# Optimization experiments

Measured on AMD Instinct MI355X. Metric: run time of the kernel, lower is better.

## Reference

```python
import jax, jax.numpy as jnp
from jax import lax
import numpy as np

COST_CLASS = 1.0
COST_BEZIER = 5.0
INF = jnp.float32(1e30)


def setup_inputs() -> dict:
    key = jax.random.key(0)
    k1, k2, k3, k4 = jax.random.split(key, 4)
    B, N, M, C = 16, 256, 256, 4096
    return {
        'pred_ctrl': jax.random.normal(k1, (B, N, 4, 2), dtype=jnp.float32),
        'pred_logits': jax.random.normal(k2, (B, N, C), dtype=jnp.float32),
        'gt_ctrl': jax.random.normal(k3, (B, M, 4, 2), dtype=jnp.float32),
        'gt_labels': jax.random.randint(k4, (B, M), 0, C, dtype=jnp.int64),
    }


def build_cost(pred_ctrl, pred_logits, gt_ctrl, gt_labels):
    B, N = pred_ctrl.shape[:2]
    M = gt_ctrl.shape[1]
    prob = jax.nn.softmax(pred_logits, axis=-1)                      # (B,N,C)
    lbl = jnp.broadcast_to(gt_labels[:, None, :], (B, N, M))          # (B,N,M)
    cost_class = -jnp.take_along_axis(prob, lbl, axis=2)              # (B,N,M)
    p = pred_ctrl.reshape(B, N, 8)
    g = gt_ctrl.reshape(B, M, 8)
    cost_bezier = jnp.sum(jnp.abs(p[:, :, None, :] - g[:, None, :, :]), axis=-1)  # L1 cdist
    return COST_CLASS * cost_class + COST_BEZIER * cost_bezier        # (B,N,M)


def lsa(cost):
    """Jonker-Volgenant shortest augmenting path, square n x n cost.
    Returns (row_ind, col_ind) matching scipy.optimize.linear_sum_assignment."""
    n = cost.shape[0]
    ar = jnp.arange(n)

    def solve_row(carry, cur_row):
        u, v, row4col, col4row = carry

        def cond(s):
            return s['sink'] < 0

        def body(s):
            i = s['i']
            SR = s['SR'].at[i].set(True)
            r = s['minVal'] + cost[i] - u[i] - v
            better = (r < s['spc']) & (~s['SC'])
            path = jnp.where(better, i, s['path'])
            spc = jnp.where(better, r, s['spc'])
            masked = jnp.where(s['SC'], INF, spc)
            j = jnp.argmin(masked).astype(jnp.int32)
            minVal = masked[j]
            SC = s['SC'].at[j].set(True)
            hit_free = row4col[j] < 0
            sink = jnp.where(hit_free, j, jnp.int32(-1))
            i_next = jnp.where(hit_free, i, row4col[j])
            return dict(i=i_next, minVal=minVal, SR=SR, SC=SC, spc=spc, path=path, sink=sink)

        init = dict(i=cur_row.astype(jnp.int32), minVal=jnp.float32(0),
                    SR=jnp.zeros(n, bool), SC=jnp.zeros(n, bool),
                    spc=jnp.full(n, INF), path=jnp.full(n, -1, jnp.int32),
                    sink=jnp.int32(-1))
        s = lax.while_loop(cond, body, init)
        minVal, SR, SC, spc, path, sink = s['minVal'], s['SR'], s['SC'], s['spc'], s['path'], s['sink']

        # dual updates
        u = u.at[cur_row].add(minVal)
        safe = jnp.clip(col4row, 0, n - 1)
        u = jnp.where(SR & (ar != cur_row), u + minVal - spc[safe], u)
        v = jnp.where(SC, v - (minVal - spc), v)

        # augment along predecessor path
        def aug_cond(t):
            return ~t['done']

        def aug_body(t):
            j = t['j']
            i = path[j]
            r4c = t['row4col'].at[j].set(i)
            j_next = t['col4row'][i]
            c4r = t['col4row'].at[i].set(j)
            return dict(j=j_next, row4col=r4c, col4row=c4r, done=(i == cur_row))

        t = lax.while_loop(aug_cond, aug_body,
                           dict(j=sink, row4col=row4col, col4row=col4row, done=jnp.bool_(False)))
        return (u, v, t['row4col'], t['col4row']), None

    init = (jnp.zeros(n, jnp.float32), jnp.zeros(n, jnp.float32),
            jnp.full(n, -1, jnp.int32), jnp.full(n, -1, jnp.int32))
    (u, v, row4col, col4row), _ = lax.scan(solve_row, init, ar)
    return ar.astype(jnp.int64), col4row.astype(jnp.int64)


_batched_lsa = jax.jit(jax.vmap(lsa))


def reference(pred_ctrl, pred_logits, gt_ctrl, gt_labels):
    C = build_cost(pred_ctrl, pred_logits, gt_ctrl, gt_labels)  # (B,N,M)
    row_ind, col_ind = _batched_lsa(C)                           # each (B,N)
    return row_ind, col_ind, C
```

## Files before the change

kernel.cpp:

```cpp
#include <hip/hip_runtime.h>

#define BATCH 16
#define NROW  256
#define MCOL  256
#define CDIM  4096
#define INF_F 1e30f
#define CROWS 144

__global__ __launch_bounds__(256)
void cost_fused_kernel(const float* __restrict__ pred_ctrl,
                       const float* __restrict__ logits,
                       const float* __restrict__ gt_ctrl,
                       const int* __restrict__ gt_labels,
                       float* __restrict__ Cout) {
    const int bn = blockIdx.x;
    const int b  = bn >> 8;
    const int t  = threadIdx.x;
    const int lane = t & 63, wave = t >> 6;
    const float* rp = logits + (size_t)bn * CDIM;

    __shared__ float part[4];
    __shared__ float smax, ssum;

    float mx = -INF_F;
    for (int c = t; c < CDIM; c += 256) mx = fmaxf(mx, rp[c]);
    for (int off = 32; off; off >>= 1) mx = fmaxf(mx, __shfl_down(mx, off));
    if (lane == 0) part[wave] = mx;
    __syncthreads();
    if (t == 0) smax = fmaxf(fmaxf(part[0], part[1]), fmaxf(part[2], part[3]));
    __syncthreads();
    mx = smax;

    float s = 0.f;
    for (int c = t; c < CDIM; c += 256) s += expf(rp[c] - mx);
    for (int off = 32; off; off >>= 1) s += __shfl_down(s, off);
    __syncthreads();
    if (lane == 0) part[wave] = s;
    __syncthreads();
    if (t == 0) ssum = part[0] + part[1] + part[2] + part[3];
    __syncthreads();

    const float rmax = smax, rsum = ssum;
    const int m = t;

    const float* pp = pred_ctrl + (size_t)bn * 8;
    const float p0 = pp[0], p1 = pp[1], p2 = pp[2], p3 = pp[3];
    const float p4 = pp[4], p5 = pp[5], p6 = pp[6], p7 = pp[7];

    const float* gp = gt_ctrl + ((size_t)b * MCOL + m) * 8;
    const float4 ga = *(const float4*)gp;
    const float4 gb = *(const float4*)(gp + 4);

    const int lbl = gt_labels[b * MCOL + m];
    const float prob = expf(rp[lbl] - rmax) / rsum;

    float cb = fabsf(p0 - ga.x);
    cb += fabsf(p1 - ga.y);
    cb += fabsf(p2 - ga.z);
    cb += fabsf(p3 - ga.w);
    cb += fabsf(p4 - gb.x);
    cb += fabsf(p5 - gb.y);
    cb += fabsf(p6 - gb.z);
    cb += fabsf(p7 - gb.w);

    Cout[(size_t)bn * MCOL + m] = -prob + 5.0f * cb;
}

__device__ __forceinline__ unsigned ordkey(float f) {
    unsigned b = __float_as_uint(f);
    return (b & 0x80000000u) ? ~b : (b | 0x80000000u);
}
__device__ __forceinline__ float unordkey(unsigned k) {
    unsigned b = (k & 0x80000000u) ? (k ^ 0x80000000u) : ~k;
    return __uint_as_float(b);
}

template<int CTRL>
__device__ __forceinline__ unsigned dpp_min_step(unsigned x) {
    const unsigned o = (unsigned)__builtin_amdgcn_update_dpp((int)x, (int)x, CTRL, 0xf, 0xf, false);
    return o < x ? o : x;
}
__device__ __forceinline__ unsigned wave_min_u32(unsigned x) {
    x = dpp_min_step<0x111>(x);
    x = dpp_min_step<0x112>(x);
    x = dpp_min_step<0x114>(x);
    x = dpp_min_step<0x118>(x);
    x = dpp_min_step<0x142>(x);
    x = dpp_min_step<0x143>(x);
    return (unsigned)__builtin_amdgcn_readlane((int)x, 63);
}

__device__ __forceinline__ float readlane_f(float x, int lane_idx) {
    return __int_as_float(__builtin_amdgcn_readlane(__float_as_int(x), lane_idx));
}
__device__ __forceinline__ float sel4f(float a0, float a1, float a2, float a3, int s) {
    float r = a0;
    r = (s == 1) ? a1 : r;
    r = (s == 2) ? a2 : r;
    r = (s == 3) ? a3 : r;
    return r;
}
__device__ __forceinline__ int sel4i(int a0, int a1, int a2, int a3, int s) {
    int r = a0;
    r = (s == 1) ? a1 : r;
    r = (s == 2) ? a2 : r;
    r = (s == 3) ? a3 : r;
    return r;
}

__global__ __launch_bounds__(64)
void lsa_kernel(const float* __restrict__ Cmat,
                float* __restrict__ out_row,
                float* __restrict__ out_col) {
    const int b = blockIdx.x;
    const int t = threadIdx.x;
    const int jb = 4 * t;
    const float* C = Cmat + (size_t)b * NROW * MCOL;

    __shared__ float Cc[CROWS][MCOL];
    __shared__ int row4col_s[MCOL];
    __shared__ int col4row_s[NROW];
    __shared__ int path_s[MCOL];
    __shared__ int queue_s[NROW];
    __shared__ int argrow_s[MCOL];
    __shared__ int nfree_s;

    float m0 = INF_F, m1 = INF_F, m2 = INF_F, m3 = INF_F;
    int   r0 = 0, r1 = 0, r2 = 0, r3 = 0;
    for (int i = 0; i < NROW; i++) {
        const float4 c4 = *(const float4*)(C + (size_t)i * MCOL + jb);
        if (i < CROWS) *(float4*)&Cc[i][jb] = c4;
        if (c4.x < m0) { m0 = c4.x; r0 = i; }
        if (c4.y < m1) { m1 = c4.y; r1 = i; }
        if (c4.z < m2) { m2 = c4.z; r2 = i; }
        if (c4.w < m3) { m3 = c4.w; r3 = i; }
    }
    float v0 = m0, v1 = m1, v2 = m2, v3 = m3;
    float u0 = 0.f, u1 = 0.f, u2 = 0.f, u3 = 0.f;

    argrow_s[jb + 0] = r0; argrow_s[jb + 1] = r1;
    argrow_s[jb + 2] = r2; argrow_s[jb + 3] = r3;
    for (int k = 0; k < 4; k++) {
        row4col_s[jb + k] = -1;
        col4row_s[jb + k] = -1;
        path_s[jb + k] = -1;
    }
    __syncthreads();

    if (t == 0) {
        for (int j = 0; j < MCOL; j++) {
            const int r = argrow_s[j];
            if (col4row_s[r] < 0) { col4row_s[r] = j; row4col_s[j] = r; }
        }
    }
    __syncthreads();

    int4 q;
    q = *(const int4*)&row4col_s[jb];
    int rc0 = q.x, rc1 = q.y, rc2 = q.z, rc3 = q.w;
    q = *(const int4*)&col4row_s[jb];
    int cr0 = q.x, cr1 = q.y, cr2 = q.z, cr3 = q.w;

    int budget = 8 * NROW;
    for (int round = 0; round < 2; round++) {
        *(int4*)&col4row_s[jb] = make_int4(cr0, cr1, cr2, cr3);
        __syncthreads();
        if (t == 0) {
            int nf = 0;
            for (int i2 = 0; i2 < NROW; i2++)
                if (col4row_s[i2] < 0) queue_s[nf++] = i2;
            nfree_s = nf;
        }
        __syncthreads();
        const int nfr = __builtin_amdgcn_readfirstlane(nfree_s);
        if (nfr == 0) break;

        for (int qi = 0; qi < nfr && budget > 0; qi++) {
            int i = __builtin_amdgcn_readfirstlane(queue_s[qi]);
            while (i >= 0 && budget > 0) {
                budget--;
                float4 c4;
                if (i < CROWS) c4 = *(const float4*)&Cc[i][jb];
                else           c4 = *(const float4*)(C + (size_t)i * MCOL + jb);
                const float d0 = c4.x - v0, d1 = c4.y - v1;
                const float d2 = c4.z - v2, d3 = c4.w - v3;
                unsigned lmin; int lslot, lrc;
                {
                    const unsigned k0 = ordkey(d0), k1 = ordkey(d1);
                    const unsigned k2 = ordkey(d2), k3 = ordkey(d3);
                    lmin = k0; lslot = 0; lrc = rc0;
                    if (k1 < lmin) { lmin = k1; lslot = 1; lrc = rc1; }
                    if (k2 < lmin) { lmin = k2; lslot = 2; lrc = rc2; }
                    if (k3 < lmin) { lmin = k3; lslot = 3; lrc = rc3; }
                }
                const unsigned g1 = wave_min_u32(lmin);
                const unsigned long long bal = __ballot(lmin == g1);
                const int w = __ffsll(bal) - 1;
                const int pk = __builtin_amdgcn_readlane(((lrc + 1) << 2) | lslot, w);
                const int j1 = 4 * w + (pk & 3);
                const int kold = (pk >> 2) - 1;
                const float mu1 = unordkey(g1);

                unsigned lmin2 = lmin;
                if (w == t) {
                    const int sl = pk & 3; unsigned k;
                    lmin2 = 0xFFFFFFFFu;
                    if (sl != 0) { k = ordkey(d0); if (k < lmin2) lmin2 = k; }
                    if (sl != 1) { k = ordkey(d1); if (k < lmin2) lmin2 = k; }
                    if (sl != 2) { k = ordkey(d2); if (k < lmin2) lmin2 = k; }
                    if (sl != 3) { k = ordkey(d3); if (k < lmin2) lmin2 = k; }
                }
                const unsigned g2 = wave_min_u32(lmin2);
                const float mu2 = unordkey(g2);

                if ((i >> 2) == t) {
                    const int s = i & 3;
                    u0 = s == 0 ? mu2 : u0; u1 = s == 1 ? mu2 : u1;
                    u2 = s == 2 ? mu2 : u2; u3 = s == 3 ? mu2 : u3;
                }
                if (w == t && mu2 > mu1) {
                    const int s = pk & 3; const float dv = mu2 - mu1;
                    v0 -= s == 0 ? dv : 0.f; v1 -= s == 1 ? dv : 0.f;
                    v2 -= s == 2 ? dv : 0.f; v3 -= s == 3 ? dv : 0.f;
                }
                if (w == t) {
                    const int s = pk & 3;
                    rc0 = s == 0 ? i : rc0; rc1 = s == 1 ? i : rc1;
                    rc2 = s == 2 ? i : rc2; rc3 = s == 3 ? i : rc3;
                }
                if ((i >> 2) == t) {
                    const int s = i & 3;
                    cr0 = s == 0 ? j1 : cr0; cr1 = s == 1 ? j1 : cr1;
                    cr2 = s == 2 ? j1 : cr2; cr3 = s == 3 ? j1 : cr3;
                }
                if (kold >= 0 && (kold >> 2) == t) {
                    const int s = kold & 3;
                    cr0 = s == 0 ? -1 : cr0; cr1 = s == 1 ? -1 : cr1;
                    cr2 = s == 2 ? -1 : cr2; cr3 = s == 3 ? -1 : cr3;
                }
                i = kold;
            }
        }
    }

    *(int4*)&col4row_s[jb] = make_int4(cr0, cr1, cr2, cr3);
    *(int4*)&row4col_s[jb] = make_int4(rc0, rc1, rc2, rc3);
    __syncthreads();
    if (t == 0) {
        int nf = 0;
        for (int i2 = 0; i2 < NROW; i2++)
            if (col4row_s[i2] < 0) queue_s[nf++] = i2;
        nfree_s = nf;
    }
    __syncthreads();

    const int nphase = __builtin_amdgcn_readfirstlane(nfree_s);
    for (int ph = 0; ph < nphase; ph++) {
        const int cur = __builtin_amdgcn_readfirstlane(queue_s[ph]);
        q = *(const int4*)&row4col_s[jb];
        rc0 = q.x; rc1 = q.y; rc2 = q.z; rc3 = q.w;

        float s0 = INF_F, s1 = INF_F, s2 = INF_F, s3 = INF_F;
        float e0 = 0.f, e1 = 0.f, e2 = 0.f, e3 = 0.f;
        int scmask = 0, srmask = 0;
        int i = cur, sink = -1;
        float minVal = 0.f;

        for (int it = 0; it < MCOL && sink < 0; it++) {
            if ((i >> 2) == t) srmask |= 1 << (i & 3);
            const float ui = readlane_f(sel4f(u0, u1, u2, u3, i & 3), i >> 2);
            float4 c4;
            if (i < CROWS) c4 = *(const float4*)&Cc[i][jb];
            else           c4 = *(const float4*)(C + (size_t)i * MCOL + jb);
            const float base = minVal - ui;
            float d;
            d = base + c4.x - v0; if (!(scmask & 1) && d < s0) { s0 = d; path_s[jb + 0] = i; }
            d = base + c4.y - v1; if (!(scmask & 2) && d < s1) { s1 = d; path_s[jb + 1] = i; }
            d = base + c4.z - v2; if (!(scmask & 4) && d < s2) { s2 = d; path_s[jb + 2] = i; }
            d = base + c4.w - v3; if (!(scmask & 8) && d < s3) { s3 = d; path_s[jb + 3] = i; }

            unsigned lmin = 0xFFFFFFFFu; int lslot = 0, lrc = -1;
            if (!(scmask & 1)) { const unsigned k = ordkey(s0); if (k < lmin) { lmin = k; lslot = 0; lrc = rc0; } }
            if (!(scmask & 2)) { const unsigned k = ordkey(s1); if (k < lmin) { lmin = k; lslot = 1; lrc = rc1; } }
            if (!(scmask & 4)) { const unsigned k = ordkey(s2); if (k < lmin) { lmin = k; lslot = 2; lrc = rc2; } }
            if (!(scmask & 8)) { const unsigned k = ordkey(s3); if (k < lmin) { lmin = k; lslot = 3; lrc = rc3; } }

            const unsigned g = wave_min_u32(lmin);
            const unsigned long long bal = __ballot(lmin == g);
            const int w = __ffsll(bal) - 1;
            const int pk = __builtin_amdgcn_readlane(((lrc + 1) << 2) | lslot, w);
            const int mj = 4 * w + (pk & 3);
            const int rc = (pk >> 2) - 1;
            minVal = unordkey(g);

            if (w == t) scmask |= 1 << (pk & 3);
            if (rc < 0) {
                sink = mj;
            } else {
                i = rc;
                if ((rc >> 2) == t) {
                    const int s = rc & 3;
                    e0 = s == 0 ? minVal : e0; e1 = s == 1 ? minVal : e1;
                    e2 = s == 2 ? minVal : e2; e3 = s == 3 ? minVal : e3;
                }
            }
        }

        if (srmask & 1) u0 += ((jb + 0) == cur) ? minVal : (minVal - e0);
        if (srmask & 2) u1 += ((jb + 1) == cur) ? minVal : (minVal - e1);
        if (srmask & 4) u2 += ((jb + 2) == cur) ? minVal : (minVal - e2);
        if (srmask & 8) u3 += ((jb + 3) == cur) ? minVal : (minVal - e3);
        if (scmask & 1) v0 -= (minVal - s0);
        if (scmask & 2) v1 -= (minVal - s1);
        if (scmask & 4) v2 -= (minVal - s2);
        if (scmask & 8) v3 -= (minVal - s3);

        __syncthreads();
        if (t == 0) {
            int j = sink;
            while (true) {
                const int ii = path_s[j];
                row4col_s[j] = ii;
                const int jn = col4row_s[ii];
                col4row_s[ii] = j;
                if (ii == cur) break;
                j = jn;
            }
        }
        __syncthreads();
    }

    for (int k = 0; k < 4; k++) {
        const int idx = jb + k;
        out_row[b * NROW + idx] = (float)idx;
        out_col[b * NROW + idx] = (float)col4row_s[idx];
    }
}

extern "C" void kernel_launch(void* const* d_in, const int* in_sizes, int n_in,
                              void* d_out, int out_size, void* d_ws, size_t ws_size,
                              hipStream_t stream) {
    const float* pred_ctrl   = (const float*)d_in[0];
    const float* pred_logits = (const float*)d_in[1];
    const float* gt_ctrl     = (const float*)d_in[2];
    const int*   gt_labels   = (const int*)d_in[3];

    float* out     = (float*)d_out;
    float* out_row = out;
    float* out_col = out + BATCH * NROW;
    float* Cout    = out + 2 * BATCH * NROW;

    cost_fused_kernel<<<BATCH * NROW, 256, 0, stream>>>(pred_ctrl, pred_logits,
                                                        gt_ctrl, gt_labels, Cout);
    lsa_kernel<<<BATCH, 64, 0, stream>>>(Cout, out_row, out_col);
}
```

Baseline: 2.134 ms.

## Replace auction/per-row augmentation with multi-source Dijkstra phases and register-resident bookkeeping

Drops the auction-style reduction pass and the per-free-row shortest augmenting path loop. Each phase now starts a multi-source Dijkstra from all currently free rows, seeding slack with a software-pipelined batched relaxation, then augments one path. Path and assignment arrays stay in registers and are read with readlane, which removes the shared-memory path array and the __syncthreads-guarded single-thread augmentation. The freed LDS allows more cost rows to be cached. The risk is that multi-source phases can pick different tie-breaks than the scipy-style reference and that each phase does a larger seeding pass.

```diff
diff --git a/kernel.cpp b/kernel.cpp
--- a/kernel.cpp
+++ b/kernel.cpp
@@ -5,7 +5,7 @@
 #define MCOL  256
 #define CDIM  4096
 #define INF_F 1e30f
-#define CROWS 144
+#define CROWS 152
 
 __global__ __launch_bounds__(256)
 void cost_fused_kernel(const float* __restrict__ pred_ctrl,
@@ -118,12 +118,9 @@
     const float* C = Cmat + (size_t)b * NROW * MCOL;
 
     __shared__ float Cc[CROWS][MCOL];
-    __shared__ int row4col_s[MCOL];
-    __shared__ int col4row_s[NROW];
-    __shared__ int path_s[MCOL];
-    __shared__ int queue_s[NROW];
     __shared__ int argrow_s[MCOL];
-    __shared__ int nfree_s;
+    __shared__ int c4r_s[NROW];
+    __shared__ int r4c_s[MCOL];
 
     float m0 = INF_F, m1 = INF_F, m2 = INF_F, m3 = INF_F;
     int   r0 = 0, r1 = 0, r2 = 0, r3 = 0;
@@ -140,201 +137,158 @@
 
     argrow_s[jb + 0] = r0; argrow_s[jb + 1] = r1;
     argrow_s[jb + 2] = r2; argrow_s[jb + 3] = r3;
-    for (int k = 0; k < 4; k++) {
-        row4col_s[jb + k] = -1;
-        col4row_s[jb + k] = -1;
-        path_s[jb + k] = -1;
-    }
+    for (int k = 0; k < 4; k++) { c4r_s[jb + k] = -1; r4c_s[jb + k] = -1; }
     __syncthreads();
 
     if (t == 0) {
         for (int j = 0; j < MCOL; j++) {
             const int r = argrow_s[j];
-            if (col4row_s[r] < 0) { col4row_s[r] = j; row4col_s[j] = r; }
+            if (c4r_s[r] < 0) { c4r_s[r] = j; r4c_s[j] = r; }
         }
     }
     __syncthreads();
 
     int4 q;
-    q = *(const int4*)&row4col_s[jb];
+    q = *(const int4*)&r4c_s[jb];
     int rc0 = q.x, rc1 = q.y, rc2 = q.z, rc3 = q.w;
-    q = *(const int4*)&col4row_s[jb];
+    q = *(const int4*)&c4r_s[jb];
     int cr0 = q.x, cr1 = q.y, cr2 = q.z, cr3 = q.w;
 
-    int budget = 8 * NROW;
-    for (int round = 0; round < 2; round++) {
-        *(int4*)&col4row_s[jb] = make_int4(cr0, cr1, cr2, cr3);
-        __syncthreads();
-        if (t == 0) {
-            int nf = 0;
-            for (int i2 = 0; i2 < NROW; i2++)
-                if (col4row_s[i2] < 0) queue_s[nf++] = i2;
-            nfree_s = nf;
-        }
-        __syncthreads();
-        const int nfr = __builtin_amdgcn_readfirstlane(nfree_s);
-        if (nfr == 0) break;
-
-        for (int qi = 0; qi < nfr && budget > 0; qi++) {
-            int i = __builtin_amdgcn_readfirstlane(queue_s[qi]);
-            while (i >= 0 && budget > 0) {
-                budget--;
-                float4 c4;
-                if (i < CROWS) c4 = *(const float4*)&Cc[i][jb];
-                else           c4 = *(const float4*)(C + (size_t)i * MCOL + jb);
-                const float d0 = c4.x - v0, d1 = c4.y - v1;
-                const float d2 = c4.z - v2, d3 = c4.w - v3;
-                unsigned lmin; int lslot, lrc;
-                {
-                    const unsigned k0 = ordkey(d0), k1 = ordkey(d1);
-                    const unsigned k2 = ordkey(d2), k3 = ordkey(d3);
-                    lmin = k0; lslot = 0; lrc = rc0;
-                    if (k1 < lmin) { lmin = k1; lslot = 1; lrc = rc1; }
-                    if (k2 < lmin) { lmin = k2; lslot = 2; lrc = rc2; }
-                    if (k3 < lmin) { lmin = k3; lslot = 3; lrc = rc3; }
-                }
-                const unsigned g1 = wave_min_u32(lmin);
-                const unsigned long long bal = __ballot(lmin == g1);
-                const int w = __ffsll(bal) - 1;
-                const int pk = __builtin_amdgcn_readlane(((lrc + 1) << 2) | lslot, w);
-                const int j1 = 4 * w + (pk & 3);
-                const int kold = (pk >> 2) - 1;
-                const float mu1 = unordkey(g1);
-
-                unsigned lmin2 = lmin;
-                if (w == t) {
-                    const int sl = pk & 3; unsigned k;
-                    lmin2 = 0xFFFFFFFFu;
-                    if (sl != 0) { k = ordkey(d0); if (k < lmin2) lmin2 = k; }
-                    if (sl != 1) { k = ordkey(d1); if (k < lmin2) lmin2 = k; }
-                    if (sl != 2) { k = ordkey(d2); if (k < lmin2) lmin2 = k; }
-                    if (sl != 3) { k = ordkey(d3); if (k < lmin2) lmin2 = k; }
-                }
-                const unsigned g2 = wave_min_u32(lmin2);
-                const float mu2 = unordkey(g2);
-
-                if ((i >> 2) == t) {
-                    const int s = i & 3;
-                    u0 = s == 0 ? mu2 : u0; u1 = s == 1 ? mu2 : u1;
-                    u2 = s == 2 ? mu2 : u2; u3 = s == 3 ? mu2 : u3;
-                }
-                if (w == t && mu2 > mu1) {
-                    const int s = pk & 3; const float dv = mu2 - mu1;
-                    v0 -= s == 0 ? dv : 0.f; v1 -= s == 1 ? dv : 0.f;
-                    v2 -= s == 2 ? dv : 0.f; v3 -= s == 3 ? dv : 0.f;
-                }
-                if (w == t) {
-                    const int s = pk & 3;
-                    rc0 = s == 0 ? i : rc0; rc1 = s == 1 ? i : rc1;
-                    rc2 = s == 2 ? i : rc2; rc3 = s == 3 ? i : rc3;
-                }
-                if ((i >> 2) == t) {
-                    const int s = i & 3;
-                    cr0 = s == 0 ? j1 : cr0; cr1 = s == 1 ? j1 : cr1;
-                    cr2 = s == 2 ? j1 : cr2; cr3 = s == 3 ? j1 : cr3;
-                }
-                if (kold >= 0 && (kold >> 2) == t) {
-                    const int s = kold & 3;
-                    cr0 = s == 0 ? -1 : cr0; cr1 = s == 1 ? -1 : cr1;
-                    cr2 = s == 2 ? -1 : cr2; cr3 = s == 3 ? -1 : cr3;
-                }
-                i = kold;
+    for (int ph = 0; ph < NROW; ph++) {
+        unsigned long long mm0 = __ballot(cr0 < 0);
+        unsigned long long mm1 = __ballot(cr1 < 0);
+        unsigned long long mm2 = __ballot(cr2 < 0);
+        unsigned long long mm3 = __ballot(cr3 < 0);
+        if (!(mm0 | mm1 | mm2 | mm3)) break;
+
+        float s0 = INF_F, s1 = INF_F, s2 = INF_F, s3 = INF_F;
+        int   p0 = -1,    p1 = -1,    p2 = -1,    p3 = -1;
+        float e0 = 0.f, e1 = 0.f, e2 = 0.f, e3 = 0.f;
+        int scmask = 0, srmask = 0;
+
+        auto next_src = [&]() -> int {
+            if (mm0) { const int l = __ffsll(mm0) - 1; mm0 &= mm0 - 1; return 4 * l + 0; }
+            if (mm1) { const int l = __ffsll(mm1) - 1; mm1 &= mm1 - 1; return 4 * l + 1; }
+            if (mm2) { const int l = __ffsll(mm2) - 1; mm2 &= mm2 - 1; return 4 * l + 2; }
+            if (mm3) { const int l = __ffsll(mm3) - 1; mm3 &= mm3 - 1; return 4 * l + 3; }
+            return -1;
+        };
+        auto relax0 = [&](int i, const float4& c4) {
+            const float ui = readlane_f(sel4f(u0, u1, u2, u3, i & 3), i >> 2);
+            float d;
+            d = c4.x - ui - v0; if (d < s0) { s0 = d; p0 = i; }
+            d = c4.y - ui - v1; if (d < s1) { s1 = d; p1 = i; }
+            d = c4.z - ui - v2; if (d < s2) { s2 = d; p2 = i; }
+            d = c4.w - ui - v3; if (d < s3) { s3 = d; p3 = i; }
+        };
+
+        {
+            const float4 z = make_float4(0.f, 0.f, 0.f, 0.f);
+            int ia0 = next_src(), ia1 = next_src(), ia2 = next_src(), ia3 = next_src();
+            float4 A0 = z, A1 = z, A2 = z, A3 = z;
+            if (ia0 >= 0) A0 = *(const float4*)(C + (size_t)ia0 * MCOL + jb);
+            if (ia1 >= 0) A1 = *(const float4*)(C + (size_t)ia1 * MCOL + jb);
+            if (ia2 >= 0) A2 = *(const float4*)(C + (size_t)ia2 * MCOL + jb);
+            if (ia3 >= 0) A3 = *(const float4*)(C + (size_t)ia3 * MCOL + jb);
+            while (ia0 >= 0) {
+                const int ib0 = next_src(), ib1 = next_src(), ib2 = next_src(), ib3 = next_src();
+                float4 B0 = z, B1 = z, B2 = z, B3 = z;
+                if (ib0 >= 0) B0 = *(const float4*)(C + (size_t)ib0 * MCOL + jb);
+                if (ib1 >= 0) B1 = *(const float4*)(C + (size_t)ib1 * MCOL + jb);
+                if (ib2 >= 0) B2 = *(const float4*)(C + (size_t)ib2 * MCOL + jb);
+                if (ib3 >= 0) B3 = *(const float4*)(C + (size_t)ib3 * MCOL + jb);
+                relax0(ia0, A0);
+                if (ia1 >= 0) relax0(ia1, A1);
+                if (ia2 >= 0) relax0(ia2, A2);
+                if (ia3 >= 0) relax0(ia3, A3);
+                ia0 = ib0; A0 = B0; ia1 = ib1; A1 = B1;
+                ia2 = ib2; A2 = B2; ia3 = ib3; A3 = B3;
             }
         }
-    }
-
-    *(int4*)&col4row_s[jb] = make_int4(cr0, cr1, cr2, cr3);
-    *(int4*)&row4col_s[jb] = make_int4(rc0, rc1, rc2, rc3);
-    __syncthreads();
-    if (t == 0) {
-        int nf = 0;
-        for (int i2 = 0; i2 < NROW; i2++)
-            if (col4row_s[i2] < 0) queue_s[nf++] = i2;
-        nfree_s = nf;
-    }
-    __syncthreads();
-
-    const int nphase = __builtin_amdgcn_readfirstlane(nfree_s);
-    for (int ph = 0; ph < nphase; ph++) {
-        const int cur = __builtin_amdgcn_readfirstlane(queue_s[ph]);
-        q = *(const int4*)&row4col_s[jb];
-        rc0 = q.x; rc1 = q.y; rc2 = q.z; rc3 = q.w;
-
-        float s0 = INF_F, s1 = INF_F, s2 = INF_F, s3 = INF_F;
-        float e0 = 0.f, e1 = 0.f, e2 = 0.f, e3 = 0.f;
-        int scmask = 0, srmask = 0;
-        int i = cur, sink = -1;
+
         float minVal = 0.f;
-
-        for (int it = 0; it < MCOL && sink < 0; it++) {
-            if ((i >> 2) == t) srmask |= 1 << (i & 3);
+        int sink = -1;
+        for (int it = 0; it < MCOL; it++) {
+            unsigned lmin = 0xFFFFFFFFu; int lslot = 0, lrc = -1;
+            if (!(scmask & 1)) { const unsigned k = ordkey(s0); if (k < lmin) { lmin = k; lslot = 0; lrc = rc0; } }
+            if (!(scmask & 2)) { const unsigned k = ordkey(s1); if (k < lmin) { lmin = k; lslot = 1; lrc = rc1; } }
+            if (!(scmask & 4)) { const unsigned k = ordkey(s2); if (k < lmin) { lmin = k; lslot = 2; lrc = rc2; } }
+            if (!(scmask & 8)) { const unsigned k = ordkey(s3); if (k < lmin) { lmin = k; lslot = 3; lrc = rc3; } }
+
+            const unsigned g = wave_min_u32(lmin);
+            const unsigned long long bal = __ballot(lmin == g);
+            const int w = __ffsll(bal) - 1;
+            const int pk = __builtin_amdgcn_readlane(((lrc + 1) << 2) | lslot, w);
+            const int mj = 4 * w + (pk & 3);
+            const int rcx = (pk >> 2) - 1;
+            minVal = unordkey(g);
+
+            if (w == t) scmask |= 1 << (pk & 3);
+            if (rcx < 0) { sink = mj; break; }
+
+            const int i = rcx;
+            if ((i >> 2) == t) {
+                const int s = i & 3;
+                srmask |= 1 << s;
+                e0 = s == 0 ? minVal : e0; e1 = s == 1 ? minVal : e1;
+                e2 = s == 2 ? minVal : e2; e3 = s == 3 ? minVal : e3;
+            }
             const float ui = readlane_f(sel4f(u0, u1, u2, u3, i & 3), i >> 2);
             float4 c4;
             if (i < CROWS) c4 = *(const float4*)&Cc[i][jb];
             else           c4 = *(const float4*)(C + (size_t)i * MCOL + jb);
             const float base = minVal - ui;
             float d;
-            d = base + c4.x - v0; if (!(scmask & 1) && d < s0) { s0 = d; path_s[jb + 0] = i; }
-            d = base + c4.y - v1; if (!(scmask & 2) && d < s1) { s1 = d; path_s[jb + 1] = i; }
-            d = base + c4.z - v2; if (!(scmask & 4) && d < s2) { s2 = d; path_s[jb + 2] = i; }
-            d = base + c4.w - v3; if (!(scmask & 8) && d < s3) { s3 = d; path_s[jb + 3] = i; }
-
-            unsigned lmin = 0xFFFFFFFFu; int lslot = 0, lrc = -1;
-            if (!(scmask & 1)) { const unsigned k = ordkey(s0); if (k < lmin) { lmin = k; lslot = 0; lrc = rc0; } }
-            if (!(scmask & 2)) { const unsigned k = ordkey(s1); if (k < lmin) { lmin = k; lslot = 1; lrc = rc1; } }
-            if (!(scmask & 4)) { const unsigned k = ordkey(s2); if (k < lmin) { lmin = k; lslot = 2; lrc = rc2; } }
-            if (!(scmask & 8)) { const unsigned k = ordkey(s3); if (k < lmin) { lmin = k; lslot = 3; lrc = rc3; } }
-
-            const unsigned g = wave_min_u32(lmin);
-            const unsigned long long bal = __ballot(lmin == g);
-            const int w = __ffsll(bal) - 1;
-            const int pk = __builtin_amdgcn_readlane(((lrc + 1) << 2) | lslot, w);
-            const int mj = 4 * w + (pk & 3);
-            const int rc = (pk >> 2) - 1;
-            minVal = unordkey(g);
-
-            if (w == t) scmask |= 1 << (pk & 3);
-            if (rc < 0) {
-                sink = mj;
-            } else {
-                i = rc;
-                if ((rc >> 2) == t) {
-                    const int s = rc & 3;
-                    e0 = s == 0 ? minVal : e0; e1 = s == 1 ? minVal : e1;
-                    e2 = s == 2 ? minVal : e2; e3 = s == 3 ? minVal : e3;
-                }
-            }
+            d = base + c4.x - v0; if (!(scmask & 1) && d < s0) { s0 = d; p0 = i; }
+            d = base + c4.y - v1; if (!(scmask & 2) && d < s1) { s1 = d; p1 = i; }
+            d = base + c4.z - v2; if (!(scmask & 4) && d < s2) { s2 = d; p2 = i; }
+            d = base + c4.w - v3; if (!(scmask & 8) && d < s3) { s3 = d; p3 = i; }
         }
 
-        if (srmask & 1) u0 += ((jb + 0) == cur) ? minVal : (minVal - e0);
-        if (srmask & 2) u1 += ((jb + 1) == cur) ? minVal : (minVal - e1);
-        if (srmask & 4) u2 += ((jb + 2) == cur) ? minVal : (minVal - e2);
-        if (srmask & 8) u3 += ((jb + 3) == cur) ? minVal : (minVal - e3);
+        if (sink < 0) break;
+
+        if (cr0 < 0) u0 += minVal;
+        if (cr1 < 0) u1 += minVal;
+        if (cr2 < 0) u2 += minVal;
+        if (cr3 < 0) u3 += minVal;
+        if (srmask & 1) u0 += minVal - e0;
+        if (srmask & 2) u1 += minVal - e1;
+        if (srmask & 4) u2 += minVal - e2;
+        if (srmask & 8) u3 += minVal - e3;
         if (scmask & 1) v0 -= (minVal - s0);
         if (scmask & 2) v1 -= (minVal - s1);
         if (scmask & 4) v2 -= (minVal - s2);
         if (scmask & 8) v3 -= (minVal - s3);
 
-        __syncthreads();
-        if (t == 0) {
-            int j = sink;
-            while (true) {
-                const int ii = path_s[j];
-                row4col_s[j] = ii;
-                const int jn = col4row_s[ii];
-                col4row_s[ii] = j;
-                if (ii == cur) break;
-                j = jn;
+        int j = sink;
+        for (int g2 = 0; g2 < NROW; g2++) {
+            const int pi = __builtin_amdgcn_readlane(
+                sel4i(p0, p1, p2, p3, j & 3), j >> 2);
+            if ((j >> 2) == t) {
+                const int s = j & 3;
+                rc0 = s == 0 ? pi : rc0; rc1 = s == 1 ? pi : rc1;
+                rc2 = s == 2 ? pi : rc2; rc3 = s == 3 ? pi : rc3;
             }
+            const int jn = __builtin_amdgcn_readlane(
+                sel4i(cr0, cr1, cr2, cr3, pi & 3), pi >> 2);
+            if ((pi >> 2) == t) {
+                const int s = pi & 3;
+                cr0 = s == 0 ? j : cr0; cr1 = s == 1 ? j : cr1;
+                cr2 = s == 2 ? j : cr2; cr3 = s == 3 ? j : cr3;
+            }
+            if (jn < 0) break;
+            j = jn;
         }
-        __syncthreads();
     }
 
-    for (int k = 0; k < 4; k++) {
-        const int idx = jb + k;
-        out_row[b * NROW + idx] = (float)idx;
-        out_col[b * NROW + idx] = (float)col4row_s[idx];
-    }
+    out_row[b * NROW + jb + 0] = (float)(jb + 0);
+    out_row[b * NROW + jb + 1] = (float)(jb + 1);
+    out_row[b * NROW + jb + 2] = (float)(jb + 2);
+    out_row[b * NROW + jb + 3] = (float)(jb + 3);
+    out_col[b * NROW + jb + 0] = (float)cr0;
+    out_col[b * NROW + jb + 1] = (float)cr1;
+    out_col[b * NROW + jb + 2] = (float)cr2;
+    out_col[b * NROW + jb + 3] = (float)cr3;
 }
 
 extern "C" void kernel_launch(void* const* d_in, const int* in_sizes, int n_in,
```

Result: slower. 3.862 ms (+81.0%).
